# Performance work log

Hardware: AMD Instinct MI355X
Metric: run time of the kernel (lower is better)

The kernel has to match this reference:

```python
import jax, jax.numpy as jnp
import numpy as np

N_NODES = 50000
N_EDGES = 800000
HID = 128
HEADS = 1
VOCAB = 1001  # input_dim + 1
OUT = 16
NEG_SLOPE = 0.2  # DGL GATv2Conv default


def setup_inputs():
    key = jax.random.key(0)
    ks = jax.random.split(key, 12)
    s = 1.0 / np.sqrt(HID)
    inp = {}
    inp['feats'] = jax.random.randint(ks[0], (N_NODES, 2), 0, VOCAB, dtype=jnp.int64)
    inp['src'] = jax.random.randint(ks[1], (N_EDGES,), 0, N_NODES, dtype=jnp.int32)
    inp['dst'] = jax.random.randint(ks[2], (N_EDGES,), 0, N_NODES, dtype=jnp.int32)
    inp['key_emb'] = jax.random.normal(ks[3], (VOCAB, HID), jnp.float32)
    inp['val_emb'] = jax.random.normal(ks[4], (VOCAB, HID), jnp.float32)
    inp['W1'] = jax.random.uniform(ks[5], (HID, HEADS * HID), jnp.float32, -s, s)
    inp['attn1'] = jax.random.uniform(ks[6], (HEADS, HID), jnp.float32, -s, s)
    inp['W2'] = jax.random.uniform(ks[7], (HID, HEADS * HID), jnp.float32, -s, s)
    inp['attn2'] = jax.random.uniform(ks[8], (HEADS, HID), jnp.float32, -s, s)
    inp['cls_w'] = jax.random.uniform(ks[9], (HID, OUT), jnp.float32, -s, s)
    return inp


def _gatv2_layer(h, W, attn, src, dst):
    # share_weights=True: one linear transform for both src and dst roles
    feat = (h @ W).reshape(N_NODES, HEADS, HID)          # [N,H,D]
    e = jax.nn.leaky_relu(feat[src] + feat[dst], NEG_SLOPE)  # [E,H,D]
    logits = jnp.einsum('ehd,hd->eh', e, attn)            # [E,H]
    # segment softmax over incoming edges of each dst node
    m = jax.ops.segment_max(logits, dst, num_segments=N_NODES)  # [N,H]
    ex = jnp.exp(logits - m[dst])
    denom = jax.ops.segment_sum(ex, dst, num_segments=N_NODES)
    a = ex / denom[dst]                                   # [E,H]
    # weighted scatter-aggregate of src features to dst nodes
    return jax.ops.segment_sum(a[:, :, None] * feat[src], dst, num_segments=N_NODES)  # [N,H,D]


def reference(feats, src, dst, key_emb, val_emb, W1, attn1, W2, attn2, cls_w):
    h = jax.nn.relu(key_emb[feats[:, 0]] + val_emb[feats[:, 1]])  # [N,HID]
    h = _gatv2_layer(h, W1, attn1, src, dst).mean(axis=1)         # mean over heads
    h = _gatv2_layer(h, W2, attn2, src, dst).mean(axis=1)
    return h @ cls_w  # [N,OUT]
```

## Files before the change

kernel.cpp:

```cpp
#include <hip/hip_runtime.h>
#include <hip/hip_fp16.h>
#include <math.h>

#define HID 128

struct h4pack { __half2 a, b; };

__device__ __forceinline__ float4 h4tof4(h4pack h) {
  float2 lo = __half22float2(h.a);
  float2 hi = __half22float2(h.b);
  return make_float4(lo.x, lo.y, hi.x, hi.y);
}

__device__ __forceinline__ h4pack f4toh4(float4 v) {
  h4pack h;
  h.a = __floats2half2_rn(v.x, v.y);
  h.b = __floats2half2_rn(v.z, v.w);
  return h;
}

__global__ __launch_bounds__(256) void zero_kernel(int4* __restrict__ p, int n4) {
  int i = blockIdx.x * 256 + threadIdx.x;
  if (i < n4) p[i] = make_int4(0, 0, 0, 0);
}

__global__ __launch_bounds__(256) void hist_kernel(
    const int* __restrict__ dst, int* __restrict__ counts,
    int* __restrict__ rank, int E) {
  int e = blockIdx.x * 256 + threadIdx.x;
  if (e < E) rank[e] = atomicAdd(&counts[dst[e]], 1);
}

__global__ __launch_bounds__(256) void partial_kernel(
    const int* __restrict__ counts, int* __restrict__ partials, int N) {
  __shared__ int s[256];
  int idx = blockIdx.x * 256 + threadIdx.x;
  int c = (idx < N) ? counts[idx] : 0;
  s[threadIdx.x] = (idx < N) ? ((c + 7) & ~7) : 0;
  __syncthreads();
  for (int o = 128; o > 0; o >>= 1) {
    if (threadIdx.x < o) s[threadIdx.x] += s[threadIdx.x + o];
    __syncthreads();
  }
  if (threadIdx.x == 0) partials[blockIdx.x] = s[0];
}

__global__ __launch_bounds__(256) void scan2_kernel(
    const int* __restrict__ partials, int* __restrict__ bases, int NB) {
  __shared__ int s[256];
  int t = threadIdx.x;
  int v0 = (t < NB) ? partials[t] : 0;
  s[t] = v0;
  __syncthreads();
  for (int o = 1; o < 256; o <<= 1) {
    int v = (t >= o) ? s[t - o] : 0;
    __syncthreads();
    s[t] += v;
    __syncthreads();
  }
  bases[t] = s[t] - v0;
}

__global__ __launch_bounds__(256) void offs_kernel(
    const int* __restrict__ counts, const int* __restrict__ bases,
    int* __restrict__ offs, int* __restrict__ csr, int N) {
  __shared__ int s[256];
  int t = threadIdx.x;
  int idx = blockIdx.x * 256 + t;
  int deg = (idx < N) ? counts[idx] : 0;
  int c = (idx < N) ? ((deg + 7) & ~7) : 0;
  s[t] = c;
  __syncthreads();
  for (int o = 1; o < 256; o <<= 1) {
    int v = (t >= o) ? s[t - o] : 0;
    __syncthreads();
    s[t] += v;
    __syncthreads();
  }
  int base = bases[blockIdx.x];
  if (idx < N) {
    int o = base + s[t] - c;
    offs[idx] = o;
    for (int k = deg; k < c; ++k) csr[o + k] = 0;
  }
  if (idx == N - 1) offs[N] = base + s[t];
}

__global__ __launch_bounds__(256) void scatter_kernel(
    const int* __restrict__ src, const int* __restrict__ dst,
    const int* __restrict__ offs, const int* __restrict__ rank,
    int* __restrict__ csr, int E) {
  int e = blockIdx.x * 256 + threadIdx.x;
  if (e >= E) return;
  csr[offs[dst[e]] + rank[e]] = src[e];
}

template <bool FUSE_EMBED>
__global__ __launch_bounds__(256) void gemm_kernel(
    const __half* __restrict__ H, const int* __restrict__ feats,
    const float* __restrict__ ke, const float* __restrict__ ve,
    const float* __restrict__ W, __half* __restrict__ F, int N, int ntiles) {
  __shared__ h4pack sW2[128 * 32];
  __shared__ float sH[32][128];
  const float4* W4 = (const float4*)W;
  for (int i = threadIdx.x; i < 128 * 32; i += 256) sW2[i] = f4toh4(W4[i]);

  int rg = threadIdx.x >> 5;
  int cg = threadIdx.x & 31;

  for (int tile = blockIdx.x; tile < ntiles; tile += gridDim.x) {
    int row0 = tile * 32;
    __syncthreads();
    for (int i = threadIdx.x; i < 32 * 32; i += 256) {
      int r = i >> 5, j = i & 31;
      int row = row0 + r;
      float4 v = make_float4(0.f, 0.f, 0.f, 0.f);
      if (row < N) {
        if (FUSE_EMBED) {
          int f0 = feats[2 * row], f1 = feats[2 * row + 1];
          float4 a = ((const float4*)(ke + (size_t)f0 * HID))[j];
          float4 b = ((const float4*)(ve + (size_t)f1 * HID))[j];
          v.x = fmaxf(a.x + b.x, 0.f);
          v.y = fmaxf(a.y + b.y, 0.f);
          v.z = fmaxf(a.z + b.z, 0.f);
          v.w = fmaxf(a.w + b.w, 0.f);
        } else {
          v = h4tof4(((const h4pack*)H)[(size_t)row * 32 + j]);
        }
      }
      ((float4*)&sH[r][0])[j] = v;
    }
    __syncthreads();

    float4 acc0 = make_float4(0.f, 0.f, 0.f, 0.f);
    float4 acc1 = acc0, acc2 = acc0, acc3 = acc0;
#pragma unroll 8
    for (int k4 = 0; k4 < 128; k4 += 4) {
      float4 h0 = *((const float4*)&sH[rg * 4 + 0][k4]);
      float4 h1 = *((const float4*)&sH[rg * 4 + 1][k4]);
      float4 h2 = *((const float4*)&sH[rg * 4 + 2][k4]);
      float4 h3 = *((const float4*)&sH[rg * 4 + 3][k4]);
      float4 w0 = h4tof4(sW2[(k4 + 0) * 32 + cg]);
      float4 w1 = h4tof4(sW2[(k4 + 1) * 32 + cg]);
      float4 w2 = h4tof4(sW2[(k4 + 2) * 32 + cg]);
      float4 w3 = h4tof4(sW2[(k4 + 3) * 32 + cg]);
#define STEP(hh, ww)                                                           \
      acc0.x = fmaf(hh##0, ww.x, acc0.x); acc0.y = fmaf(hh##0, ww.y, acc0.y);  \
      acc0.z = fmaf(hh##0, ww.z, acc0.z); acc0.w = fmaf(hh##0, ww.w, acc0.w);  \
      acc1.x = fmaf(hh##1, ww.x, acc1.x); acc1.y = fmaf(hh##1, ww.y, acc1.y);  \
      acc1.z = fmaf(hh##1, ww.z, acc1.z); acc1.w = fmaf(hh##1, ww.w, acc1.w);  \
      acc2.x = fmaf(hh##2, ww.x, acc2.x); acc2.y = fmaf(hh##2, ww.y, acc2.y);  \
      acc2.z = fmaf(hh##2, ww.z, acc2.z); acc2.w = fmaf(hh##2, ww.w, acc2.w);  \
      acc3.x = fmaf(hh##3, ww.x, acc3.x); acc3.y = fmaf(hh##3, ww.y, acc3.y);  \
      acc3.z = fmaf(hh##3, ww.z, acc3.z); acc3.w = fmaf(hh##3, ww.w, acc3.w)
      { float hx0 = h0.x, hx1 = h1.x, hx2 = h2.x, hx3 = h3.x; STEP(hx, w0); }
      { float hx0 = h0.y, hx1 = h1.y, hx2 = h2.y, hx3 = h3.y; STEP(hx, w1); }
      { float hx0 = h0.z, hx1 = h1.z, hx2 = h2.z, hx3 = h3.z; STEP(hx, w2); }
      { float hx0 = h0.w, hx1 = h1.w, hx2 = h2.w, hx3 = h3.w; STEP(hx, w3); }
#undef STEP
    }
    int r0 = row0 + rg * 4;
    if (r0 + 0 < N) ((h4pack*)F)[(size_t)(r0 + 0) * 32 + cg] = f4toh4(acc0);
    if (r0 + 1 < N) ((h4pack*)F)[(size_t)(r0 + 1) * 32 + cg] = f4toh4(acc1);
    if (r0 + 2 < N) ((h4pack*)F)[(size_t)(r0 + 2) * 32 + cg] = f4toh4(acc2);
    if (r0 + 3 < N) ((h4pack*)F)[(size_t)(r0 + 3) * 32 + cg] = f4toh4(acc3);
  }
}

__device__ __forceinline__ float dot4f(const float4& f, const float4& fd,
                                       const float4& a6, const float4& a4) {
  float t, p;
  t = f.x + fd.x; p = a6.x * t;         p = fmaf(a4.x, fabsf(t), p);
  t = f.y + fd.y; p = fmaf(a6.y, t, p); p = fmaf(a4.y, fabsf(t), p);
  t = f.z + fd.z; p = fmaf(a6.z, t, p); p = fmaf(a4.z, fabsf(t), p);
  t = f.w + fd.w; p = fmaf(a6.w, t, p); p = fmaf(a4.w, fabsf(t), p);
  return p;
}

__global__ __launch_bounds__(256) void gat_kernel(
    const __half* __restrict__ F, const int* __restrict__ offs,
    const int* __restrict__ counts, const int* __restrict__ csr,
    const float* __restrict__ attn, __half* __restrict__ Hout, int N) {
  int node = blockIdx.x * 8 + (threadIdx.x >> 5);
  if (node >= N) return;
  int q = threadIdx.x & 31;
  int lane = threadIdx.x & 63;
  const h4pack* F4h = (const h4pack*)F;
  float4 fd = h4tof4(F4h[(size_t)node * 32 + q]);
  float4 av = ((const float4*)attn)[q];
  float4 a6, a4;
  a6.x = 0.6f * av.x; a6.y = 0.6f * av.y; a6.z = 0.6f * av.z; a6.w = 0.6f * av.w;
  a4.x = 0.4f * av.x; a4.y = 0.4f * av.y; a4.z = 0.4f * av.z; a4.w = 0.4f * av.w;
  int ib = (lane & 32) << 2;
  bool b1 = (q & 1) != 0;
  bool b2 = (q & 2) != 0;
  bool b4 = (q & 4) != 0;

  int beg = offs[node];
  int cnt = counts[node];
  float l = 0.f;
  float4 acc = make_float4(0.f, 0.f, 0.f, 0.f);

  int nit = (cnt + 7) >> 3;
  const int* cp = csr + beg;
  for (int it = 0; it < nit; ++it) {
    const int4* qp = (const int4*)(cp + 8 * it);
    int4 sa = qp[0];
    int4 sb = qp[1];
    float4 fa0 = h4tof4(F4h[(size_t)sa.x * 32 + q]);
    float4 fa1 = h4tof4(F4h[(size_t)sa.y * 32 + q]);
    float4 fa2 = h4tof4(F4h[(size_t)sa.z * 32 + q]);
    float4 fa3 = h4tof4(F4h[(size_t)sa.w * 32 + q]);
    float4 fb0 = h4tof4(F4h[(size_t)sb.x * 32 + q]);
    float4 fb1 = h4tof4(F4h[(size_t)sb.y * 32 + q]);
    float4 fb2 = h4tof4(F4h[(size_t)sb.z * 32 + q]);
    float4 fb3 = h4tof4(F4h[(size_t)sb.w * 32 + q]);
    int rem = cnt - 8 * it;
    float p0 = dot4f(fa0, fd, a6, a4);
    float p1 = (1 < rem) ? dot4f(fa1, fd, a6, a4) : -INFINITY;
    float p2 = (2 < rem) ? dot4f(fa2, fd, a6, a4) : -INFINITY;
    float p3 = (3 < rem) ? dot4f(fa3, fd, a6, a4) : -INFINITY;
    float p4 = (4 < rem) ? dot4f(fb0, fd, a6, a4) : -INFINITY;
    float p5 = (5 < rem) ? dot4f(fb1, fd, a6, a4) : -INFINITY;
    float p6 = (6 < rem) ? dot4f(fb2, fd, a6, a4) : -INFINITY;
    float p7 = (7 < rem) ? dot4f(fb3, fd, a6, a4) : -INFINITY;
    float u0 = p0 + __shfl_xor(p0, 1, 64);
    float u1 = p1 + __shfl_xor(p1, 1, 64);
    float u2 = p2 + __shfl_xor(p2, 1, 64);
    float u3 = p3 + __shfl_xor(p3, 1, 64);
    float u4 = p4 + __shfl_xor(p4, 1, 64);
    float u5 = p5 + __shfl_xor(p5, 1, 64);
    float u6 = p6 + __shfl_xor(p6, 1, 64);
    float u7 = p7 + __shfl_xor(p7, 1, 64);
    float c0 = b1 ? u1 : u0;
    float c1 = b1 ? u3 : u2;
    float c2 = b1 ? u5 : u4;
    float c3 = b1 ? u7 : u6;
    float d0 = c0 + __shfl_xor(c0, 2, 64);
    float d1 = c1 + __shfl_xor(c1, 2, 64);
    float d2 = c2 + __shfl_xor(c2, 2, 64);
    float d3 = c3 + __shfl_xor(c3, 2, 64);
    float w0 = b2 ? d1 : d0;
    float w1 = b2 ? d3 : d2;
    float x0 = w0 + __shfl_xor(w0, 4, 64);
    float x1 = w1 + __shfl_xor(w1, 4, 64);
    float r = b4 ? x1 : x0;
    r += __shfl_xor(r, 8, 64);
    r += __shfl_xor(r, 16, 64);
    float ex = __expf(r);
    int exi = __float_as_int(ex);
    float e0 = __int_as_float(__builtin_amdgcn_ds_bpermute(ib +  0, exi));
    float e1 = __int_as_float(__builtin_amdgcn_ds_bpermute(ib +  4, exi));
    float e2 = __int_as_float(__builtin_amdgcn_ds_bpermute(ib +  8, exi));
    float e3 = __int_as_float(__builtin_amdgcn_ds_bpermute(ib + 12, exi));
    float e4 = __int_as_float(__builtin_amdgcn_ds_bpermute(ib + 16, exi));
    float e5 = __int_as_float(__builtin_amdgcn_ds_bpermute(ib + 20, exi));
    float e6 = __int_as_float(__builtin_amdgcn_ds_bpermute(ib + 24, exi));
    float e7 = __int_as_float(__builtin_amdgcn_ds_bpermute(ib + 28, exi));
    l += ((e0 + e1) + (e2 + e3)) + ((e4 + e5) + (e6 + e7));
    acc.x = fmaf(e0, fa0.x, acc.x); acc.x = fmaf(e1, fa1.x, acc.x);
    acc.x = fmaf(e2, fa2.x, acc.x); acc.x = fmaf(e3, fa3.x, acc.x);
    acc.x = fmaf(e4, fb0.x, acc.x); acc.x = fmaf(e5, fb1.x, acc.x);
    acc.x = fmaf(e6, fb2.x, acc.x); acc.x = fmaf(e7, fb3.x, acc.x);
    acc.y = fmaf(e0, fa0.y, acc.y); acc.y = fmaf(e1, fa1.y, acc.y);
    acc.y = fmaf(e2, fa2.y, acc.y); acc.y = fmaf(e3, fa3.y, acc.y);
    acc.y = fmaf(e4, fb0.y, acc.y); acc.y = fmaf(e5, fb1.y, acc.y);
    acc.y = fmaf(e6, fb2.y, acc.y); acc.y = fmaf(e7, fb3.y, acc.y);
    acc.z = fmaf(e0, fa0.z, acc.z); acc.z = fmaf(e1, fa1.z, acc.z);
    acc.z = fmaf(e2, fa2.z, acc.z); acc.z = fmaf(e3, fa3.z, acc.z);
    acc.z = fmaf(e4, fb0.z, acc.z); acc.z = fmaf(e5, fb1.z, acc.z);
    acc.z = fmaf(e6, fb2.z, acc.z); acc.z = fmaf(e7, fb3.z, acc.z);
    acc.w = fmaf(e0, fa0.w, acc.w); acc.w = fmaf(e1, fa1.w, acc.w);
    acc.w = fmaf(e2, fa2.w, acc.w); acc.w = fmaf(e3, fa3.w, acc.w);
    acc.w = fmaf(e4, fb0.w, acc.w); acc.w = fmaf(e5, fb1.w, acc.w);
    acc.w = fmaf(e6, fb2.w, acc.w); acc.w = fmaf(e7, fb3.w, acc.w);
  }
  float inv = (l > 0.f) ? 1.f / l : 0.f;
  acc.x *= inv; acc.y *= inv; acc.z *= inv; acc.w *= inv;
  ((h4pack*)Hout)[(size_t)node * 32 + q] = f4toh4(acc);
}

__global__ __launch_bounds__(256) void classify_kernel(
    const __half* __restrict__ H, const float* __restrict__ Wc,
    float* __restrict__ out, int N) {
  __shared__ float sW[HID * 16];
  __shared__ float sH[16][132];
  for (int i = threadIdx.x; i < HID * 16; i += 256) sW[i] = Wc[i];
  int row0 = blockIdx.x * 16;
  for (int i = threadIdx.x; i < 16 * 32; i += 256) {
    int r = i >> 5, j = i & 31;
    int row = row0 + r;
    float4 v = make_float4(0.f, 0.f, 0.f, 0.f);
    if (row < N) v = h4tof4(((const h4pack*)H)[(size_t)row * 32 + j]);
    ((float4*)&sH[r][0])[j] = v;
  }
  __syncthreads();
  int r = threadIdx.x >> 4;
  int c = threadIdx.x & 15;
  float acc = 0.f;
#pragma unroll 8
  for (int k = 0; k < HID; ++k) acc = fmaf(sH[r][k], sW[k * 16 + c], acc);
  int row = row0 + r;
  if (row < N) out[(size_t)row * 16 + c] = acc;
}

extern "C" void kernel_launch(void* const* d_in, const int* in_sizes, int n_in,
                              void* d_out, int out_size, void* d_ws, size_t ws_size,
                              hipStream_t stream) {
  const int* feats     = (const int*)d_in[0];
  const int* src       = (const int*)d_in[1];
  const int* dst       = (const int*)d_in[2];
  const float* key_emb = (const float*)d_in[3];
  const float* val_emb = (const float*)d_in[4];
  const float* W1      = (const float*)d_in[5];
  const float* attn1   = (const float*)d_in[6];
  const float* W2      = (const float*)d_in[7];
  const float* attn2   = (const float*)d_in[8];
  const float* cls_w   = (const float*)d_in[9];

  int N = in_sizes[0] / 2;
  int E = in_sizes[1];
  int NB = (N + 255) / 256;
  int ntiles = (N + 31) / 32;

  int Np = (N + 3) & ~3;
  int Ep = (E + 3) & ~3;
  char* ws = (char*)d_ws;
  __half* fbuf  = (__half*)ws;
  __half* hbuf  = (__half*)(ws + (size_t)Np * HID * 2);
  int* counts   = (int*)(ws + (size_t)Np * HID * 4);
  int* offs     = counts + Np;
  int* rank     = offs + Np + 4;
  int* csr      = rank + Ep;
  int* partials = csr + Ep + 8 * (size_t)Np;
  int* bases    = partials + 256;

  zero_kernel<<<(Np / 4 + 255) / 256, 256, 0, stream>>>((int4*)counts, Np / 4);

  hist_kernel<<<(E + 255) / 256, 256, 0, stream>>>(dst, counts, rank, E);
  partial_kernel<<<NB, 256, 0, stream>>>(counts, partials, N);
  scan2_kernel<<<1, 256, 0, stream>>>(partials, bases, NB);
  offs_kernel<<<NB, 256, 0, stream>>>(counts, bases, offs, csr, N);
  scatter_kernel<<<(E + 255) / 256, 256, 0, stream>>>(src, dst, offs, rank, csr, E);

  gemm_kernel<true><<<768, 256, 0, stream>>>(
      nullptr, feats, key_emb, val_emb, W1, fbuf, N, ntiles);
  gat_kernel<<<(N + 7) / 8, 256, 0, stream>>>(
      fbuf, offs, counts, csr, attn1, hbuf, N);
  gemm_kernel<false><<<768, 256, 0, stream>>>(
      hbuf, nullptr, nullptr, nullptr, W2, fbuf, N, ntiles);
  gat_kernel<<<(N + 7) / 8, 256, 0, stream>>>(
      fbuf, offs, counts, csr, attn2, hbuf, N);

  classify_kernel<<<(N + 15) / 16, 256, 0, stream>>>(hbuf, cls_w, (float*)d_out, N);
}
```

Baseline: 226.7 us.

## Replace scalar FMA GEMM with MFMA f16 matrix-core kernel and split embedding

Replaces the LDS-tiled scalar FP32 FMA GEMM with a kernel using the 16x16x32 f16 MFMA instruction. A and transposed W are loaded straight from global memory, with no shared-memory staging. The embedding gather and ReLU move into a separate kernel that writes an fp16 buffer, and a small prep kernel transposes and converts W1 and W2 to fp16. This removes the FMA-bound inner loop. In exchange it adds three extra launches, an extra round trip of the embedding buffer through memory, and scattered 2-byte output stores.

```diff
diff --git a/kernel.cpp b/kernel.cpp
--- a/kernel.cpp
+++ b/kernel.cpp
@@ -3,6 +3,9 @@
 #include <math.h>
 
 #define HID 128
+
+typedef _Float16 half8 __attribute__((ext_vector_type(8)));
+typedef float floatx4 __attribute__((ext_vector_type(4)));
 
 struct h4pack { __half2 a, b; };
 
@@ -95,75 +98,63 @@
   csr[offs[dst[e]] + rank[e]] = src[e];
 }
 
-template <bool FUSE_EMBED>
-__global__ __launch_bounds__(256) void gemm_kernel(
-    const __half* __restrict__ H, const int* __restrict__ feats,
-    const float* __restrict__ ke, const float* __restrict__ ve,
-    const float* __restrict__ W, __half* __restrict__ F, int N, int ntiles) {
-  __shared__ h4pack sW2[128 * 32];
-  __shared__ float sH[32][128];
-  const float4* W4 = (const float4*)W;
-  for (int i = threadIdx.x; i < 128 * 32; i += 256) sW2[i] = f4toh4(W4[i]);
-
-  int rg = threadIdx.x >> 5;
-  int cg = threadIdx.x & 31;
-
-  for (int tile = blockIdx.x; tile < ntiles; tile += gridDim.x) {
-    int row0 = tile * 32;
-    __syncthreads();
-    for (int i = threadIdx.x; i < 32 * 32; i += 256) {
-      int r = i >> 5, j = i & 31;
-      int row = row0 + r;
-      float4 v = make_float4(0.f, 0.f, 0.f, 0.f);
-      if (row < N) {
-        if (FUSE_EMBED) {
-          int f0 = feats[2 * row], f1 = feats[2 * row + 1];
-          float4 a = ((const float4*)(ke + (size_t)f0 * HID))[j];
-          float4 b = ((const float4*)(ve + (size_t)f1 * HID))[j];
-          v.x = fmaxf(a.x + b.x, 0.f);
-          v.y = fmaxf(a.y + b.y, 0.f);
-          v.z = fmaxf(a.z + b.z, 0.f);
-          v.w = fmaxf(a.w + b.w, 0.f);
-        } else {
-          v = h4tof4(((const h4pack*)H)[(size_t)row * 32 + j]);
-        }
-      }
-      ((float4*)&sH[r][0])[j] = v;
+__global__ __launch_bounds__(256) void embed_kernel(
+    const int* __restrict__ feats, const float* __restrict__ ke,
+    const float* __restrict__ ve, __half* __restrict__ h0, int N) {
+  int gid = blockIdx.x * 256 + threadIdx.x;
+  int n = gid >> 4, j = gid & 15;
+  if (n >= N) return;
+  int f0 = feats[2 * n], f1 = feats[2 * n + 1];
+  const float4* a4 = (const float4*)(ke + (size_t)f0 * HID) + j * 2;
+  const float4* b4 = (const float4*)(ve + (size_t)f1 * HID) + j * 2;
+  float4 a0 = a4[0], a1 = a4[1], b0 = b4[0], b1 = b4[1];
+  float4 v0, v1;
+  v0.x = fmaxf(a0.x + b0.x, 0.f); v0.y = fmaxf(a0.y + b0.y, 0.f);
+  v0.z = fmaxf(a0.z + b0.z, 0.f); v0.w = fmaxf(a0.w + b0.w, 0.f);
+  v1.x = fmaxf(a1.x + b1.x, 0.f); v1.y = fmaxf(a1.y + b1.y, 0.f);
+  v1.z = fmaxf(a1.z + b1.z, 0.f); v1.w = fmaxf(a1.w + b1.w, 0.f);
+  h4pack* out = (h4pack*)h0 + (size_t)n * 32 + j * 2;
+  out[0] = f4toh4(v0);
+  out[1] = f4toh4(v1);
+}
+
+__global__ __launch_bounds__(256) void wprep_kernel(
+    const float* __restrict__ W, __half* __restrict__ Wt) {
+  int t = blockIdx.x * 256 + threadIdx.x;
+  int k = t >> 7, c = t & 127;
+  Wt[(size_t)c * HID + k] = __float2half(W[t]);
+}
+
+__global__ __launch_bounds__(256) void gemm_mfma_kernel(
+    const __half* __restrict__ A, const __half* __restrict__ Wt,
+    __half* __restrict__ F, int N) {
+  int w = threadIdx.x >> 6;
+  int lane = threadIdx.x & 63;
+  int r = lane & 15, g = lane >> 4;
+  int row0 = blockIdx.x * 64 + w * 16;
+  if (row0 >= N) return;
+  int arow = row0 + r;
+  if (arow >= N) arow = N - 1;
+  const half8* Ap = (const half8*)(A + (size_t)arow * HID + g * 8);
+  half8 a0 = Ap[0];
+  half8 a1 = Ap[4];
+  half8 a2 = Ap[8];
+  half8 a3 = Ap[12];
+#pragma unroll
+  for (int ct = 0; ct < 8; ++ct) {
+    const half8* Bp = (const half8*)(Wt + (size_t)(ct * 16 + r) * HID + g * 8);
+    half8 b0 = Bp[0], b1 = Bp[4], b2 = Bp[8], b3 = Bp[12];
+    floatx4 c = {0.f, 0.f, 0.f, 0.f};
+    c = __builtin_amdgcn_mfma_f32_16x16x32_f16(a0, b0, c, 0, 0, 0);
+    c = __builtin_amdgcn_mfma_f32_16x16x32_f16(a1, b1, c, 0, 0, 0);
+    c = __builtin_amdgcn_mfma_f32_16x16x32_f16(a2, b2, c, 0, 0, 0);
+    c = __builtin_amdgcn_mfma_f32_16x16x32_f16(a3, b3, c, 0, 0, 0);
+    int col = ct * 16 + r;
+#pragma unroll
+    for (int reg = 0; reg < 4; ++reg) {
+      int row = row0 + g * 4 + reg;
+      if (row < N) F[(size_t)row * HID + col] = __float2half(c[reg]);
     }
-    __syncthreads();
-
-    float4 acc0 = make_float4(0.f, 0.f, 0.f, 0.f);
-    float4 acc1 = acc0, acc2 = acc0, acc3 = acc0;
-#pragma unroll 8
-    for (int k4 = 0; k4 < 128; k4 += 4) {
-      float4 h0 = *((const float4*)&sH[rg * 4 + 0][k4]);
-      float4 h1 = *((const float4*)&sH[rg * 4 + 1][k4]);
-      float4 h2 = *((const float4*)&sH[rg * 4 + 2][k4]);
-      float4 h3 = *((const float4*)&sH[rg * 4 + 3][k4]);
-      float4 w0 = h4tof4(sW2[(k4 + 0) * 32 + cg]);
-      float4 w1 = h4tof4(sW2[(k4 + 1) * 32 + cg]);
-      float4 w2 = h4tof4(sW2[(k4 + 2) * 32 + cg]);
-      float4 w3 = h4tof4(sW2[(k4 + 3) * 32 + cg]);
-#define STEP(hh, ww)                                                           \
-      acc0.x = fmaf(hh##0, ww.x, acc0.x); acc0.y = fmaf(hh##0, ww.y, acc0.y);  \
-      acc0.z = fmaf(hh##0, ww.z, acc0.z); acc0.w = fmaf(hh##0, ww.w, acc0.w);  \
-      acc1.x = fmaf(hh##1, ww.x, acc1.x); acc1.y = fmaf(hh##1, ww.y, acc1.y);  \
-      acc1.z = fmaf(hh##1, ww.z, acc1.z); acc1.w = fmaf(hh##1, ww.w, acc1.w);  \
-      acc2.x = fmaf(hh##2, ww.x, acc2.x); acc2.y = fmaf(hh##2, ww.y, acc2.y);  \
-      acc2.z = fmaf(hh##2, ww.z, acc2.z); acc2.w = fmaf(hh##2, ww.w, acc2.w);  \
-      acc3.x = fmaf(hh##3, ww.x, acc3.x); acc3.y = fmaf(hh##3, ww.y, acc3.y);  \
-      acc3.z = fmaf(hh##3, ww.z, acc3.z); acc3.w = fmaf(hh##3, ww.w, acc3.w)
-      { float hx0 = h0.x, hx1 = h1.x, hx2 = h2.x, hx3 = h3.x; STEP(hx, w0); }
-      { float hx0 = h0.y, hx1 = h1.y, hx2 = h2.y, hx3 = h3.y; STEP(hx, w1); }
-      { float hx0 = h0.z, hx1 = h1.z, hx2 = h2.z, hx3 = h3.z; STEP(hx, w2); }
-      { float hx0 = h0.w, hx1 = h1.w, hx2 = h2.w, hx3 = h3.w; STEP(hx, w3); }
-#undef STEP
-    }
-    int r0 = row0 + rg * 4;
-    if (r0 + 0 < N) ((h4pack*)F)[(size_t)(r0 + 0) * 32 + cg] = f4toh4(acc0);
-    if (r0 + 1 < N) ((h4pack*)F)[(size_t)(r0 + 1) * 32 + cg] = f4toh4(acc1);
-    if (r0 + 2 < N) ((h4pack*)F)[(size_t)(r0 + 2) * 32 + cg] = f4toh4(acc2);
-    if (r0 + 3 < N) ((h4pack*)F)[(size_t)(r0 + 3) * 32 + cg] = f4toh4(acc3);
   }
 }
 
@@ -321,14 +312,16 @@
   int N = in_sizes[0] / 2;
   int E = in_sizes[1];
   int NB = (N + 255) / 256;
-  int ntiles = (N + 31) / 32;
 
   int Np = (N + 3) & ~3;
   int Ep = (E + 3) & ~3;
   char* ws = (char*)d_ws;
   __half* fbuf  = (__half*)ws;
   __half* hbuf  = (__half*)(ws + (size_t)Np * HID * 2);
-  int* counts   = (int*)(ws + (size_t)Np * HID * 4);
+  __half* ebuf  = (__half*)(ws + (size_t)Np * HID * 4);
+  __half* Wt1   = (__half*)(ws + (size_t)Np * HID * 6);
+  __half* Wt2   = Wt1 + HID * HID;
+  int* counts   = (int*)(Wt2 + HID * HID);
   int* offs     = counts + Np;
   int* rank     = offs + Np + 4;
   int* csr      = rank + Ep;
@@ -343,12 +336,16 @@
   offs_kernel<<<NB, 256, 0, stream>>>(counts, bases, offs, csr, N);
   scatter_kernel<<<(E + 255) / 256, 256, 0, stream>>>(src, dst, offs, rank, csr, E);
 
-  gemm_kernel<true><<<768, 256, 0, stream>>>(
-      nullptr, feats, key_emb, val_emb, W1, fbuf, N, ntiles);
+  wprep_kernel<<<64, 256, 0, stream>>>(W1, Wt1);
+  wprep_kernel<<<64, 256, 0, stream>>>(W2, Wt2);
+  embed_kernel<<<((size_t)N * 16 + 255) / 256, 256, 0, stream>>>(
+      feats, key_emb, val_emb, ebuf, N);
+
+  int gblocks = (N + 63) / 64;
+  gemm_mfma_kernel<<<gblocks, 256, 0, stream>>>(ebuf, Wt1, fbuf, N);
   gat_kernel<<<(N + 7) / 8, 256, 0, stream>>>(
       fbuf, offs, counts, csr, attn1, hbuf, N);
-  gemm_kernel<false><<<768, 256, 0, stream>>>(
-      hbuf, nullptr, nullptr, nullptr, W2, fbuf, N, ntiles);
+  gemm_mfma_kernel<<<gblocks, 256, 0, stream>>>(hbuf, Wt2, fbuf, N);
   gat_kernel<<<(N + 7) / 8, 256, 0, stream>>>(
       fbuf, offs, counts, csr, attn2, hbuf, N);
 
```

New measurement: 205.4 us. 1.1x faster.
